# Optimization experiments

Hardware: AMD Instinct MI355X
Metric: run time of the kernel (lower is better)

The kernel has to match this reference:

```python
import jax, jax.numpy as jnp
import numpy as np

C_IN = 128   # pair channel dim
H = 4        # heads
DH = 32      # per-head dim (c_hidden // no_heads = 128 // 4)
R = 96       # low-rank bias rank (hard-coded self.Rank)
N = 384      # sequence length (pair rep is N x N)
S_DIM = 449  # s_inputs feature dim (c_in + 449 into bias MLPs)
MLP_H = 256  # bias MLP hidden width
EPS = 1e-5


def setup_inputs() -> dict:
    key = jax.random.key(0)
    ks = jax.random.split(key, 16)
    w = lambda k, shp, s=0.02: (jax.random.normal(k, shp) * s).astype(jnp.float32)
    return {
        "x": jax.random.normal(ks[0], (N, N, C_IN), dtype=jnp.float32),
        "s_inputs": jax.random.normal(ks[1], (N, S_DIM), dtype=jnp.float32),
        "ln_gamma": jnp.ones((C_IN,), jnp.float32),
        "ln_beta": jnp.zeros((C_IN,), jnp.float32),
        # q flashbias MLP (Linear->Tanh->Linear->Tanh->Linear, no bias)
        "Wq1": w(ks[2], (C_IN + S_DIM, MLP_H)),
        "Wq2": w(ks[3], (MLP_H, MLP_H)),
        "Wq3": w(ks[4], (MLP_H, H * R)),
        # k flashbias MLP
        "Wk1": w(ks[5], (C_IN + S_DIM, MLP_H)),
        "Wk2": w(ks[6], (MLP_H, MLP_H)),
        "Wk3": w(ks[7], (MLP_H, H * R)),
        # OpenFold-style gated Attention params
        "Wq_att": w(ks[8], (C_IN, H * DH)),
        "Wk_att": w(ks[9], (C_IN, H * DH)),
        "Wv_att": w(ks[10], (C_IN, H * DH)),
        "Wg": w(ks[11], (C_IN, H * DH)),
        "bg": jnp.zeros((H * DH,), jnp.float32),
        "Wo": w(ks[12], (H * DH, C_IN)),
        "bo": jnp.zeros((C_IN,), jnp.float32),
        "id": 10,  # id < 16 -> low-rank flashbias path
    }


def _layer_norm(x, gamma, beta):
    mu = jnp.mean(x, axis=-1, keepdims=True)
    var = jnp.var(x, axis=-1, keepdims=True)
    return (x - mu) * jax.lax.rsqrt(var + EPS) * gamma + beta


def _bias_mlp(z, W1, W2, W3):
    # [N, C+449] -> [N, H*R] -> [1, H, N, R]
    h = jnp.tanh(jnp.tanh(z @ W1) @ W2) @ W3
    return jnp.transpose(h.reshape(N, H, R), (1, 0, 2))[None]


def reference(x, s_inputs, ln_gamma, ln_beta, Wq1, Wq2, Wq3, Wk1, Wk2, Wk3,
              Wq_att, Wk_att, Wv_att, Wg, bg, Wo, bo, id=10):
    # starting=True, eval mode, s_inputs given, id < 16 -> low-rank bias path
    x = _layer_norm(x, ln_gamma, ln_beta)                       # [N, N, C]

    # low-rank triangle-bias factors (shared across rows, broadcast over dim 0)
    q_bias = _bias_mlp(jnp.concatenate([x.mean(1), s_inputs], -1), Wq1, Wq2, Wq3)  # [1,H,N,R]
    k_bias = _bias_mlp(jnp.concatenate([x.mean(0), s_inputs], -1), Wk1, Wk2, Wk3)  # [1,H,N,R]

    # multi-head attention over the last sequence axis, per row
    def heads(z, W):  # [N, N, C] -> [N, H, N, DH]
        return jnp.transpose((z @ W).reshape(N, N, H, DH), (0, 2, 1, 3))

    q = heads(x, Wq_att) * (1.0 / np.sqrt(DH)).astype(np.float32)
    k = heads(x, Wk_att)
    v = heads(x, Wv_att)

    scores = jnp.einsum("ihqd,ihkd->ihqk", q, k)                # [N,H,N,N]
    scores = scores + jnp.einsum("bhqr,bhkr->bhqk", q_bias, k_bias)  # broadcast over rows
    a = jax.nn.softmax(scores, axis=-1)

    o = jnp.einsum("ihqk,ihkd->ihqd", a, v)                     # [N,H,N,DH]
    o = jnp.transpose(o, (0, 2, 1, 3)).reshape(N, N, H * DH)
    g = jax.nn.sigmoid(x @ Wg + bg)                              # gating
    out = (g * o) @ Wo + bo                                      # [N, N, C]
    return out
```

## Files before the change

### kernel.cpp

```cpp
#include <hip/hip_runtime.h>
#include <cstdint>
#include <cstddef>

typedef _Float16 f16;
typedef __attribute__((ext_vector_type(2))) _Float16 f16x2;
typedef __attribute__((ext_vector_type(4))) _Float16 f16x4;
typedef __attribute__((ext_vector_type(8))) _Float16 f16x8;
typedef __attribute__((ext_vector_type(4))) float f32x4;

#define MFMA_16x16x32(a,b,c) __builtin_amdgcn_mfma_f32_16x16x32_f16((a),(b),(c),0,0,0)
#define MFMA_16x16x16(a,b,c) __builtin_amdgcn_mfma_f32_16x16x16f16((a),(b),(c),0,0,0)

#define NSEQ 384
#define CIN 128
#define NH 4
#define DHD 32
#define RNK 96
#define SDIM 449
#define MHID 256
#define NN (NSEQ*NSEQ)

#define KPAD 608
#define ZSTR 616
#define HSTR 264
#define OFF_W1 0
#define SZ_W1 (MHID*KPAD)
#define OFF_W2 (2*SZ_W1)
#define SZ_W2 (MHID*MHID)
#define OFF_W3 (OFF_W2 + 2*SZ_W2)
#define SZ_W3 ((NH*RNK)*MHID)
#define WMLP_TOT (OFF_W3 + 2*SZ_W3)

__global__ __launch_bounds__(256) void k_convert(const float* __restrict__ Wq, const float* __restrict__ Wk,
    const float* __restrict__ Wv, const float* __restrict__ Wg, const float* __restrict__ Wo,
    f16* __restrict__ W4T, f16* __restrict__ WoT) {
  int idx = blockIdx.x*256 + threadIdx.x;
  int c = idx >> 7, kk = idx & 127;
  if (c < 512) {
    int mat = c >> 7, cc = c & 127;
    const float* src = mat==0 ? Wq : (mat==1 ? Wk : (mat==2 ? Wv : Wg));
    W4T[c*CIN + kk] = (f16)src[kk*CIN + cc];
  } else {
    int cc = c - 512;
    WoT[cc*CIN + kk] = (f16)Wo[kk*CIN + cc];
  }
}

__global__ __launch_bounds__(256) void k_convert2(const float* __restrict__ Wq1, const float* __restrict__ Wq2,
    const float* __restrict__ Wq3, const float* __restrict__ Wk1, const float* __restrict__ Wk2,
    const float* __restrict__ Wk3, f16* __restrict__ wmlp) {
  int idx = blockIdx.x*256 + threadIdx.x;
  float val;
  if (idx < OFF_W2) {
    int m = idx / SZ_W1, r = idx - m*SZ_W1;
    int c = r / KPAD, kk = r - c*KPAD;
    const float* src = m ? Wk1 : Wq1;
    val = (kk < SDIM + CIN) ? src[kk*MHID + c] : 0.f;
  } else if (idx < OFF_W3) {
    int r = idx - OFF_W2;
    int m = r >> 16, rr = r & 65535;
    int c = rr >> 8, kk = rr & 255;
    const float* src = m ? Wk2 : Wq2;
    val = src[kk*MHID + c];
  } else {
    int r = idx - OFF_W3;
    int m = r / SZ_W3, rr = r - m*SZ_W3;
    int c = rr >> 8, kk = rr & 255;
    const float* src = m ? Wk3 : Wq3;
    val = src[kk*(NH*RNK) + c];
  }
  wmlp[idx] = (f16)val;
}

__global__ __launch_bounds__(256) void k_ln(const float* __restrict__ x, const float* __restrict__ gamma,
    const float* __restrict__ beta, f16* __restrict__ xn, float* __restrict__ rowm) {
  int b = blockIdx.x;
  int i = b >> 2, jbase = (b & 3) * 96;
  int t = threadIdx.x, wave = t >> 6, lane = t & 63;
  int half = lane >> 5, l31 = lane & 31;
  int c0 = l31 * 4;
  __shared__ float racc[CIN];
  if (t < CIN) racc[t] = 0.f;
  float4 g4 = *(const float4*)&gamma[c0];
  float4 b4 = *(const float4*)&beta[c0];
  float a0=0,a1=0,a2=0,a3=0;
  __syncthreads();
  for (int it = 0; it < 12; ++it) {
    int j = jbase + it*8 + wave*2 + half;
    const float4 v = *(const float4*)&x[(size_t)(i*NSEQ + j)*CIN + c0];
    float s = (v.x+v.y)+(v.z+v.w);
    float ss = (v.x*v.x+v.y*v.y)+(v.z*v.z+v.w*v.w);
#pragma unroll
    for (int off = 16; off >= 1; off >>= 1) { s += __shfl_xor(s, off); ss += __shfl_xor(ss, off); }
    float mean = s * (1.0f/CIN);
    float var = ss * (1.0f/CIN) - mean*mean;
    float rs = rsqrtf(var + 1e-5f);
    float y0 = (v.x-mean)*rs*g4.x + b4.x;
    float y1 = (v.y-mean)*rs*g4.y + b4.y;
    float y2 = (v.z-mean)*rs*g4.z + b4.z;
    float y3 = (v.w-mean)*rs*g4.w + b4.w;
    f16x4 w; w[0]=(f16)y0; w[1]=(f16)y1; w[2]=(f16)y2; w[3]=(f16)y3;
    *(f16x4*)&xn[(size_t)(i*NSEQ + j)*CIN + c0] = w;
    a0+=y0; a1+=y1; a2+=y2; a3+=y3;
  }
  atomicAdd(&racc[c0], a0); atomicAdd(&racc[c0+1], a1);
  atomicAdd(&racc[c0+2], a2); atomicAdd(&racc[c0+3], a3);
  __syncthreads();
  if (t < CIN) atomicAdd(&rowm[i*CIN + t], racc[t] * (1.0f/NSEQ));
}

__global__ __launch_bounds__(256) void k_colmean(const f16* __restrict__ xn, float* __restrict__ colm) {
  int j = blockIdx.x; int t = threadIdx.x;
  int c = t & 127, half = t >> 7;
  float acc = 0.f;
  int i0 = half*192;
#pragma unroll 4
  for (int ii = i0; ii < i0 + 192; ++ii)
    acc += (float)xn[(size_t)(ii*NSEQ + j)*CIN + c];
  __shared__ float sb[256];
  sb[t] = acc;
  __syncthreads();
  if (t < 128) colm[j*CIN + t] = (sb[t] + sb[t+128]) * (1.0f/NSEQ);
}

__global__ __launch_bounds__(256) void k_mlp2(const float* __restrict__ rowm, const float* __restrict__ colm,
    const float* __restrict__ sinp, const f16* __restrict__ wmlp,
    float* __restrict__ qbT, float* __restrict__ kbT) {
  int b = blockIdx.x;
  bool isQ = b < 12;
  int r0 = (isQ ? b : b - 12) * 32;
  const float* mean = isQ ? rowm : colm;
  const f16* W1T = wmlp + (isQ ? 0 : SZ_W1);
  const f16* W2T = wmlp + OFF_W2 + (isQ ? 0 : SZ_W2);
  const f16* W3T = wmlp + OFF_W3 + (isQ ? 0 : SZ_W3);
  float* outp = isQ ? qbT : kbT;
  int t = threadIdx.x, wave = t >> 6, lane = t & 63;
  int l15 = lane & 15, quad = lane >> 4;
  int rt = wave & 1, ch = wave >> 1;

  __shared__ __align__(16) f16 z[32*ZSTR];
  __shared__ __align__(16) f16 hbuf[2][32*HSTR];

  for (int idx = t; idx < 32*KPAD; idx += 256) {
    int row = idx / KPAD, u = idx - row*KPAD;
    float v;
    if (u < CIN) v = mean[(r0+row)*CIN + u];
    else if (u < CIN + SDIM) v = sinp[(r0+row)*SDIM + (u - CIN)];
    else v = 0.f;
    z[row*ZSTR + u] = (f16)v;
  }
  __syncthreads();

  {
    f32x4 acc[8];
#pragma unroll
    for (int c = 0; c < 8; ++c) acc[c] = (f32x4){0,0,0,0};
    for (int ks = 0; ks < 19; ++ks) {
      f16x8 af = *(const f16x8*)&z[(rt*16 + l15)*ZSTR + ks*32 + quad*8];
#pragma unroll
      for (int c = 0; c < 8; ++c) {
        f16x8 bf = *(const f16x8*)&W1T[(size_t)((ch*8 + c)*16 + l15)*KPAD + ks*32 + quad*8];
        acc[c] = MFMA_16x16x32(af, bf, acc[c]);
      }
    }
#pragma unroll
    for (int c = 0; c < 8; ++c) {
      int col = (ch*8 + c)*16 + l15;
#pragma unroll
      for (int r = 0; r < 4; ++r) {
        float th = 1.f - 2.f/(1.f + __expf(2.f*acc[c][r]));
        hbuf[0][(rt*16 + quad*4 + r)*HSTR + col] = (f16)th;
      }
    }
  }
  __syncthreads();

  {
    f32x4 acc[8];
#pragma unroll
    for (int c = 0; c < 8; ++c) acc[c] = (f32x4){0,0,0,0};
    for (int ks = 0; ks < 8; ++ks) {
      f16x8 af = *(const f16x8*)&hbuf[0][(rt*16 + l15)*HSTR + ks*32 + quad*8];
#pragma unroll
      for (int c = 0; c < 8; ++c) {
        f16x8 bf = *(const f16x8*)&W2T[(size_t)((ch*8 + c)*16 + l15)*MHID + ks*32 + quad*8];
        acc[c] = MFMA_16x16x32(af, bf, acc[c]);
      }
    }
#pragma unroll
    for (int c = 0; c < 8; ++c) {
      int col = (ch*8 + c)*16 + l15;
#pragma unroll
      for (int r = 0; r < 4; ++r) {
        float th = 1.f - 2.f/(1.f + __expf(2.f*acc[c][r]));
        hbuf[1][(rt*16 + quad*4 + r)*HSTR + col] = (f16)th;
      }
    }
  }
  __syncthreads();

  {
    f32x4 acc[12];
#pragma unroll
    for (int c = 0; c < 12; ++c) acc[c] = (f32x4){0,0,0,0};
    for (int ks = 0; ks < 8; ++ks) {
      f16x8 af = *(const f16x8*)&hbuf[1][(rt*16 + l15)*HSTR + ks*32 + quad*8];
#pragma unroll
      for (int c = 0; c < 12; ++c) {
        f16x8 bf = *(const f16x8*)&W3T[(size_t)((ch*12 + c)*16 + l15)*MHID + ks*32 + quad*8];
        acc[c] = MFMA_16x16x32(af, bf, acc[c]);
      }
    }
#pragma unroll
    for (int c = 0; c < 12; ++c) {
      int o = (ch*12 + c)*16 + l15;
#pragma unroll
      for (int r = 0; r < 4; ++r)
        outp[o*NSEQ + r0 + rt*16 + quad*4 + r] = acc[c][r];
    }
  }
}

__global__ __launch_bounds__(128) void k_bias(const float* __restrict__ qbT, const float* __restrict__ kbT,
    float* __restrict__ bias4) {
  int b = blockIdx.x;
  int h = b / 96, kg = b - h*96;
  int t = threadIdx.x;
  __shared__ float4 kr[RNK];
  if (t < RNK) kr[t] = *(const float4*)&kbT[(size_t)(h*RNK + t)*NSEQ + kg*4];
  __syncthreads();
  float acc[3][4];
#pragma unroll
  for (int m = 0; m < 3; ++m)
#pragma unroll
    for (int r = 0; r < 4; ++r) acc[m][r] = 0.f;
  for (int r = 0; r < RNK; ++r) {
    float4 kv = kr[r];
    const float* qrow = qbT + (size_t)(h*RNK + r)*NSEQ;
    float q0 = qrow[t], q1 = qrow[t+128], q2 = qrow[t+256];
    acc[0][0]+=q0*kv.x; acc[0][1]+=q0*kv.y; acc[0][2]+=q0*kv.z; acc[0][3]+=q0*kv.w;
    acc[1][0]+=q1*kv.x; acc[1][1]+=q1*kv.y; acc[1][2]+=q1*kv.z; acc[1][3]+=q1*kv.w;
    acc[2][0]+=q2*kv.x; acc[2][1]+=q2*kv.y; acc[2][2]+=q2*kv.z; acc[2][3]+=q2*kv.w;
  }
#pragma unroll
  for (int m = 0; m < 3; ++m) {
    int q = t + m*128;
    f32x4 w; w[0]=acc[m][0]; w[1]=acc[m][1]; w[2]=acc[m][2]; w[3]=acc[m][3];
    *(f32x4*)&bias4[((size_t)b*NSEQ + q)*4] = w;
  }
}

__global__ __launch_bounds__(256) void k_proj(const f16* __restrict__ xn, const f16* __restrict__ W4T,
    const float* __restrict__ bg, f16* __restrict__ qb, f16* __restrict__ kb, f16* __restrict__ vb,
    f16* __restrict__ gb) {
  int b = blockIdx.x; int mb = b >> 2, nb = b & 3;
  int t = threadIdx.x, wave = t >> 6, lane = t & 63;
  int l15 = lane & 15, quad = lane >> 4;
  __shared__ __align__(16) f16 As[128*128];
  __shared__ __align__(16) f16 Bs[128*128];
  int Mbase = mb*128;
  for (int p = 0; p < 8; ++p) {
    int c = p*256 + t; int row = c >> 4, ci = c & 15;
    int sw = (ci ^ (row & 15)) * 8;
    *(f16x8*)&As[row*128 + sw] = *(const f16x8*)&xn[(size_t)(Mbase + row)*CIN + ci*8];
    *(f16x8*)&Bs[row*128 + sw] = *(const f16x8*)&W4T[(size_t)(nb*128 + row)*CIN + ci*8];
  }
  __syncthreads();
  int m0 = wave*32;
  f16x8 af[2][4];
#pragma unroll
  for (int mt = 0; mt < 2; ++mt)
#pragma unroll
    for (int kt = 0; kt < 4; ++kt)
      af[mt][kt] = *(const f16x8*)&As[(m0 + mt*16 + l15)*128 + ((kt*4 + quad) ^ l15)*8];
  int i = mb/3, j0 = (mb - (mb/3)*3)*128 + m0;
#pragma unroll
  for (int ct = 0; ct < 8; ++ct) {
    f32x4 acc0 = (f32x4){0,0,0,0}, acc1 = (f32x4){0,0,0,0};
#pragma unroll
    for (int kt = 0; kt < 4; ++kt) {
      f16x8 bf = *(const f16x8*)&Bs[(ct*16 + l15)*128 + ((kt*4 + quad) ^ l15)*8];
      acc0 = MFMA_16x16x32(af[0][kt], bf, acc0);
      acc1 = MFMA_16x16x32(af[1][kt], bf, acc1);
    }
    int col = nb*128 + ct*16 + l15;
    int cc = col & 127;
    int hh = cc >> 5, d = cc & 31;
    if (nb == 3) {
      float bgv = bg[cc];
#pragma unroll
      for (int mt = 0; mt < 2; ++mt) {
        f32x4 a = mt ? acc1 : acc0;
#pragma unroll
        for (int r = 0; r < 4; ++r) {
          int jj = j0 + mt*16 + quad*4 + r;
          float sg = 1.0f/(1.0f + __expf(-(a[r] + bgv)));
          gb[(size_t)(i*NSEQ + jj)*CIN + cc] = (f16)sg;
        }
      }
    } else {
      f16* dstb = nb==0 ? qb : (nb==1 ? kb : vb);
      float scale = nb==0 ? 0.17677669529663687f : 1.0f;
#pragma unroll
      for (int mt = 0; mt < 2; ++mt) {
        f32x4 a = mt ? acc1 : acc0;
#pragma unroll
        for (int r = 0; r < 4; ++r) {
          int jj = j0 + mt*16 + quad*4 + r;
          dstb[((size_t)(i*NH + hh)*NSEQ + jj)*DHD + d] = (f16)(a[r]*scale);
        }
      }
    }
  }
}

__global__ __launch_bounds__(256) void k_attn(const f16* __restrict__ qg, const f16* __restrict__ kg,
    const f16* __restrict__ vg, const float* __restrict__ bias4, f16* __restrict__ og) {
  int b = blockIdx.x; int h = b & 3; int i = b >> 2;
  int t = threadIdx.x; int wave = t >> 6; int lane = t & 63;
  int l15 = lane & 15, quad = lane >> 4;
  __shared__ __align__(16) f16 Ks[NSEQ*40];
  __shared__ __align__(16) f16 Vs[NSEQ*36];
  size_t base = (size_t)(i*NH + h) * NSEQ * DHD;
  for (int p = 0; p < 6; ++p) {
    int c = p*256 + t; int row = c >> 2, ci = c & 3;
    *(f16x8*)&Ks[row*40 + ci*8] = *(const f16x8*)&kg[base + row*DHD + ci*8];
  }
  for (int p = 0; p < 12; ++p) {
    int c = p*256 + t; int row = c >> 3, ci = c & 7;
    *(f16x4*)&Vs[row*36 + ci*4] = *(const f16x4*)&vg[base + row*DHD + ci*4];
  }
  int qt0 = wave*6;
  f16x8 qf[6];
#pragma unroll
  for (int s = 0; s < 6; ++s)
    qf[s] = *(const f16x8*)&qg[base + (size_t)((qt0+s)*16 + l15)*DHD + quad*8];
  f32x4 oa[6][2];
  float lsum[6];
#pragma unroll
  for (int s = 0; s < 6; ++s) { lsum[s] = 0.f; oa[s][0] = (f32x4){0,0,0,0}; oa[s][1] = (f32x4){0,0,0,0}; }
  __syncthreads();
  for (int kt = 0; kt < 24; ++kt) {
    f16x8 kf = *(const f16x8*)&Ks[(kt*16 + l15)*40 + quad*8];
    int vbase = (kt*16 + quad*4)*36 + l15;
    f16x4 vf0, vf1;
#pragma unroll
    for (int jj = 0; jj < 4; ++jj) { vf0[jj] = Vs[vbase + jj*36]; vf1[jj] = Vs[vbase + jj*36 + 16]; }
    const float* bp = bias4 + (((size_t)h*96 + kt*4 + quad)*NSEQ + qt0*16 + l15)*4;
    f32x4 cb[6];
#pragma unroll
    for (int s = 0; s < 6; ++s) cb[s] = *(const f32x4*)(bp + s*64);
#pragma unroll
    for (int s = 0; s < 6; ++s) {
      f32x4 st = MFMA_16x16x32(kf, qf[s], cb[s]);
      float p0 = __expf(st[0]), p1 = __expf(st[1]), p2 = __expf(st[2]), p3 = __expf(st[3]);
      lsum[s] += (p0 + p1) + (p2 + p3);
      f16x4 pa; pa[0]=(f16)p0; pa[1]=(f16)p1; pa[2]=(f16)p2; pa[3]=(f16)p3;
      oa[s][0] = MFMA_16x16x16(pa, vf0, oa[s][0]);
      oa[s][1] = MFMA_16x16x16(pa, vf1, oa[s][1]);
    }
  }
#pragma unroll
  for (int s = 0; s < 6; ++s) {
    float lf = lsum[s];
    lf += __shfl_xor(lf, 16);
    lf += __shfl_xor(lf, 32);
    float inv = 1.0f / lf;
#pragma unroll
    for (int r = 0; r < 4; ++r) {
      float invr = __shfl(inv, quad*4 + r);
      int qrow = (qt0+s)*16 + quad*4 + r;
      size_t ob = (size_t)(i*NSEQ + qrow)*(NH*DHD) + h*DHD;
      og[ob + l15]      = (f16)(oa[s][0][r] * invr);
      og[ob + 16 + l15] = (f16)(oa[s][1][r] * invr);
    }
  }
}

__global__ __launch_bounds__(256) void k_final(const f16* __restrict__ gb, const f16* __restrict__ ob,
    const f16* __restrict__ WoT, const float* __restrict__ bo, float* __restrict__ out) {
  int mb = blockIdx.x;
  int t = threadIdx.x, wave = t >> 6, lane = t & 63;
  int l15 = lane & 15, quad = lane >> 4;
  __shared__ __align__(16) f16 As[128*128];
  __shared__ __align__(16) f16 Bs[128*128];
  int Mbase = mb*128;
  for (int p = 0; p < 8; ++p) {
    int c = p*256 + t; int row = c >> 4, ci = c & 15;
    int sw = (ci ^ (row & 15)) * 8;
    f16x8 gv = *(const f16x8*)&gb[(size_t)(Mbase + row)*CIN + ci*8];
    f16x8 ov = *(const f16x8*)&ob[(size_t)(Mbase + row)*CIN + ci*8];
    *(f16x8*)&As[row*128 + sw] = gv*ov;
    *(f16x8*)&Bs[row*128 + sw] = *(const f16x8*)&WoT[row*CIN + ci*8];
  }
  __syncthreads();
  int m0 = wave*32;
  f16x8 af[2][4];
#pragma unroll
  for (int mt = 0; mt < 2; ++mt)
#pragma unroll
    for (int kt = 0; kt < 4; ++kt)
      af[mt][kt] = *(const f16x8*)&As[(m0 + mt*16 + l15)*128 + ((kt*4 + quad) ^ l15)*8];
#pragma unroll
  for (int ct = 0; ct < 8; ++ct) {
    f32x4 acc0 = (f32x4){0,0,0,0}, acc1 = (f32x4){0,0,0,0};
#pragma unroll
    for (int kt = 0; kt < 4; ++kt) {
      f16x8 bf = *(const f16x8*)&Bs[(ct*16 + l15)*128 + ((kt*4 + quad) ^ l15)*8];
      acc0 = MFMA_16x16x32(af[0][kt], bf, acc0);
      acc1 = MFMA_16x16x32(af[1][kt], bf, acc1);
    }
    float bov = bo[ct*16 + l15];
#pragma unroll
    for (int mt = 0; mt < 2; ++mt) {
      f32x4 a = mt ? acc1 : acc0;
#pragma unroll
      for (int r = 0; r < 4; ++r) {
        int mrow = Mbase + m0 + mt*16 + quad*4 + r;
        out[(size_t)mrow*CIN + ct*16 + l15] = a[r] + bov;
      }
    }
  }
}

extern "C" void kernel_launch(void* const* d_in, const int* in_sizes, int n_in,
                              void* d_out, int out_size, void* d_ws, size_t ws_size,
                              hipStream_t stream) {
  (void)in_sizes; (void)n_in; (void)out_size; (void)ws_size;
  const float* x    = (const float*)d_in[0];
  const float* sinp = (const float*)d_in[1];
  const float* gam  = (const float*)d_in[2];
  const float* bet  = (const float*)d_in[3];
  const float* Wq1  = (const float*)d_in[4];
  const float* Wq2  = (const float*)d_in[5];
  const float* Wq3  = (const float*)d_in[6];
  const float* Wk1  = (const float*)d_in[7];
  const float* Wk2  = (const float*)d_in[8];
  const float* Wk3  = (const float*)d_in[9];
  const float* Wqa  = (const float*)d_in[10];
  const float* Wka  = (const float*)d_in[11];
  const float* Wva  = (const float*)d_in[12];
  const float* Wg   = (const float*)d_in[13];
  const float* bg   = (const float*)d_in[14];
  const float* Wo   = (const float*)d_in[15];
  const float* bo   = (const float*)d_in[16];
  float* out = (float*)d_out;

  char* w = (char*)d_ws;
  auto carve = [&](size_t bytes) { char* p = w; w += (bytes + 255) & ~(size_t)255; return p; };
  f16*   xn    = (f16*)carve((size_t)NN*CIN*2);
  f16*   qb    = (f16*)carve((size_t)NN*CIN*2);
  f16*   kb    = (f16*)carve((size_t)NN*CIN*2);
  f16*   vb    = (f16*)carve((size_t)NN*CIN*2);
  f16*   gbuf  = (f16*)carve((size_t)NN*CIN*2);
  float* bias4 = (float*)carve((size_t)NH*NSEQ*NSEQ*4);
  float* rowm  = (float*)carve((size_t)NSEQ*CIN*4);
  float* colm  = (float*)carve((size_t)NSEQ*CIN*4);
  float* qbT   = (float*)carve((size_t)(NH*RNK)*NSEQ*4);
  float* kbT   = (float*)carve((size_t)(NH*RNK)*NSEQ*4);
  f16*   W4T   = (f16*)carve((size_t)512*CIN*2);
  f16*   WoT   = (f16*)carve((size_t)CIN*CIN*2);
  f16*   wmlp  = (f16*)carve((size_t)WMLP_TOT*2);
  f16*   obuf  = xn;

  hipMemsetAsync(rowm, 0, (size_t)NSEQ*CIN*4, stream);
  k_convert<<<320, 256, 0, stream>>>(Wqa, Wka, Wva, Wg, Wo, W4T, WoT);
  k_convert2<<<WMLP_TOT/256, 256, 0, stream>>>(Wq1, Wq2, Wq3, Wk1, Wk2, Wk3, wmlp);
  k_ln<<<NSEQ*4, 256, 0, stream>>>(x, gam, bet, xn, rowm);
  k_colmean<<<NSEQ, 256, 0, stream>>>(xn, colm);
  k_mlp2<<<24, 256, 0, stream>>>(rowm, colm, sinp, wmlp, qbT, kbT);
  k_bias<<<NH*96, 128, 0, stream>>>(qbT, kbT, bias4);
  k_proj<<<4608, 256, 0, stream>>>(xn, W4T, bg, qb, kb, vb, gbuf);
  k_attn<<<NH*NSEQ, 256, 0, stream>>>(qb, kb, vb, bias4, obuf);
  k_final<<<1152, 256, 0, stream>>>(gbuf, obuf, WoT, bo, out);
}
```

Baseline: 458.5 us.

## Fold log2e into scores, use exp2, read K/V from global, reorder attention blocks

Pre-scales the query projection and the low-rank bias by log2(e) so the attention softmax can use the raw exp2 instruction instead of __expf. The attention kernel drops its LDS staging of K and V and the block barrier, loading K and V fragments straight from global memory through incremented pointers. Block indexing is changed so consecutive blocks share a head, which should improve cache reuse of the bias table. A launch-bounds occupancy hint is added. The trade-off is strided, uncoalesced global V loads (scalar f16 at stride DHD) in place of shared-memory reads.

```diff
diff --git a/kernel.cpp b/kernel.cpp
--- a/kernel.cpp
+++ b/kernel.cpp
@@ -19,6 +19,7 @@
 #define SDIM 449
 #define MHID 256
 #define NN (NSEQ*NSEQ)
+#define LOG2E 1.4426950408889634f
 
 #define KPAD 608
 #define ZSTR 616
@@ -245,7 +246,7 @@
 #pragma unroll
   for (int m = 0; m < 3; ++m) {
     int q = t + m*128;
-    f32x4 w; w[0]=acc[m][0]; w[1]=acc[m][1]; w[2]=acc[m][2]; w[3]=acc[m][3];
+    f32x4 w; w[0]=acc[m][0]*LOG2E; w[1]=acc[m][1]*LOG2E; w[2]=acc[m][2]*LOG2E; w[3]=acc[m][3]*LOG2E;
     *(f32x4*)&bias4[((size_t)b*NSEQ + q)*4] = w;
   }
 }
@@ -300,7 +301,7 @@
       }
     } else {
       f16* dstb = nb==0 ? qb : (nb==1 ? kb : vb);
-      float scale = nb==0 ? 0.17677669529663687f : 1.0f;
+      float scale = nb==0 ? 0.25503576722f : 1.0f;
 #pragma unroll
       for (int mt = 0; mt < 2; ++mt) {
         f32x4 a = mt ? acc1 : acc0;
@@ -314,22 +315,12 @@
   }
 }
 
-__global__ __launch_bounds__(256) void k_attn(const f16* __restrict__ qg, const f16* __restrict__ kg,
+__global__ __launch_bounds__(256, 4) void k_attn(const f16* __restrict__ qg, const f16* __restrict__ kg,
     const f16* __restrict__ vg, const float* __restrict__ bias4, f16* __restrict__ og) {
-  int b = blockIdx.x; int h = b & 3; int i = b >> 2;
+  int b = blockIdx.x; int h = b / NSEQ; int i = b - h*NSEQ;
   int t = threadIdx.x; int wave = t >> 6; int lane = t & 63;
   int l15 = lane & 15, quad = lane >> 4;
-  __shared__ __align__(16) f16 Ks[NSEQ*40];
-  __shared__ __align__(16) f16 Vs[NSEQ*36];
   size_t base = (size_t)(i*NH + h) * NSEQ * DHD;
-  for (int p = 0; p < 6; ++p) {
-    int c = p*256 + t; int row = c >> 2, ci = c & 3;
-    *(f16x8*)&Ks[row*40 + ci*8] = *(const f16x8*)&kg[base + row*DHD + ci*8];
-  }
-  for (int p = 0; p < 12; ++p) {
-    int c = p*256 + t; int row = c >> 3, ci = c & 7;
-    *(f16x4*)&Vs[row*36 + ci*4] = *(const f16x4*)&vg[base + row*DHD + ci*4];
-  }
   int qt0 = wave*6;
   f16x8 qf[6];
 #pragma unroll
@@ -339,21 +330,25 @@
   float lsum[6];
 #pragma unroll
   for (int s = 0; s < 6; ++s) { lsum[s] = 0.f; oa[s][0] = (f32x4){0,0,0,0}; oa[s][1] = (f32x4){0,0,0,0}; }
-  __syncthreads();
+  const f16* kp = kg + base + (size_t)l15*DHD + quad*8;
+  const f16* vp = vg + base + (size_t)(quad*4)*DHD + l15;
+  const float* bp = bias4 + (((size_t)h*96 + quad)*NSEQ + qt0*16 + l15)*4;
   for (int kt = 0; kt < 24; ++kt) {
-    f16x8 kf = *(const f16x8*)&Ks[(kt*16 + l15)*40 + quad*8];
-    int vbase = (kt*16 + quad*4)*36 + l15;
+    f16x8 kf = *(const f16x8*)kp;
     f16x4 vf0, vf1;
 #pragma unroll
-    for (int jj = 0; jj < 4; ++jj) { vf0[jj] = Vs[vbase + jj*36]; vf1[jj] = Vs[vbase + jj*36 + 16]; }
-    const float* bp = bias4 + (((size_t)h*96 + kt*4 + quad)*NSEQ + qt0*16 + l15)*4;
+    for (int jj = 0; jj < 4; ++jj) { vf0[jj] = vp[jj*DHD]; vf1[jj] = vp[jj*DHD + 16]; }
     f32x4 cb[6];
 #pragma unroll
     for (int s = 0; s < 6; ++s) cb[s] = *(const f32x4*)(bp + s*64);
+    kp += 16*DHD; vp += 16*DHD; bp += 4*NSEQ*4;
 #pragma unroll
     for (int s = 0; s < 6; ++s) {
       f32x4 st = MFMA_16x16x32(kf, qf[s], cb[s]);
-      float p0 = __expf(st[0]), p1 = __expf(st[1]), p2 = __expf(st[2]), p3 = __expf(st[3]);
+      float p0 = __builtin_amdgcn_exp2f(st[0]);
+      float p1 = __builtin_amdgcn_exp2f(st[1]);
+      float p2 = __builtin_amdgcn_exp2f(st[2]);
+      float p3 = __builtin_amdgcn_exp2f(st[3]);
       lsum[s] += (p0 + p1) + (p2 + p3);
       f16x4 pa; pa[0]=(f16)p0; pa[1]=(f16)p1; pa[2]=(f16)p2; pa[3]=(f16)p3;
       oa[s][0] = MFMA_16x16x16(pa, vf0, oa[s][0]);
```

Result: faster. 445.2 us (-2.9%).
